# Performance work log

Measured on AMD Instinct MI355X. Metric: run time of the kernel, lower is better.

Reference implementation:

```python
import jax, jax.numpy as jnp
import numpy as np

V, D, H, L, FF, NC = 32000, 512, 8, 4, 2048, 10
HD = D // H
EPS = 1e-5


def _layernorm(x, g, b):
    m = jnp.mean(x, axis=-1, keepdims=True)
    v = jnp.mean((x - m) ** 2, axis=-1, keepdims=True)
    return (x - m) * jax.lax.rsqrt(v + EPS) * g + b


def _pos_encoding(T, d):
    pos = jnp.arange(T, dtype=jnp.float32)[:, None]
    div = jnp.exp(jnp.arange(0, d, 2, dtype=jnp.float32) * (-np.log(10000.0) / d))
    pe = jnp.zeros((T, d), dtype=jnp.float32)
    pe = pe.at[:, 0::2].set(jnp.sin(pos * div))
    pe = pe.at[:, 1::2].set(jnp.cos(pos * div))
    return pe


def setup_inputs() -> dict:
    key = jax.random.key(0)
    ks = iter(jax.random.split(key, 32))
    n = lambda shape, s=0.02: jax.random.normal(next(ks), shape, dtype=jnp.float32) * s
    inp = {
        "tokens": jax.random.randint(next(ks), (8, 1024), 0, V),
        "emb": n((V, D), 1.0),
        # attention projections, stored (in, out) so y = x @ W + b
        "Wq": n((L, D, D)), "bq": jnp.zeros((L, D)),
        "Wk": n((L, D, D)), "bk": jnp.zeros((L, D)),
        "Wv": n((L, D, D)), "bv": jnp.zeros((L, D)),
        "Wo": n((L, D, D)), "bo": jnp.zeros((L, D)),
        "ln1_g": jnp.ones((L, D)), "ln1_b": jnp.zeros((L, D)),
        "ln2_g": jnp.ones((L, D)), "ln2_b": jnp.zeros((L, D)),
        "W1": n((L, D, FF)), "b1": jnp.zeros((L, FF)),
        "W2": n((L, FF, D)), "b2": jnp.zeros((L, D)),
        "heavy_w": n((D, D)), "heavy_b": jnp.zeros((D,)),
        "heavy_a1": n((D, D)), "heavy_a2": n((D, D)),
        "norm_g": jnp.ones((D,)), "norm_b": jnp.zeros((D,)),
        "cls_W": n((D, NC)), "cls_b": jnp.zeros((NC,)),
    }
    return inp


def reference(tokens, emb, Wq, bq, Wk, bk, Wv, bv, Wo, bo,
              ln1_g, ln1_b, ln2_g, ln2_b, W1, b1, W2, b2,
              heavy_w, heavy_b, heavy_a1, heavy_a2,
              norm_g, norm_b, cls_W, cls_b):
    B, T = tokens.shape
    x = emb[tokens] + _pos_encoding(T, D)[None]  # [B,T,D]
    scale = 1.0 / np.sqrt(HD)
    for l in range(L):
        # attention block (pre-norm)
        h = _layernorm(x, ln1_g[l], ln1_b[l])
        q = (h @ Wq[l] + bq[l]).reshape(B, T, H, HD)
        k = (h @ Wk[l] + bk[l]).reshape(B, T, H, HD)
        v = (h @ Wv[l] + bv[l]).reshape(B, T, H, HD)
        scores = jnp.einsum("bqhd,bkhd->bhqk", q, k) * scale
        attn = jax.nn.softmax(scores, axis=-1)
        o = jnp.einsum("bhqk,bkhd->bqhd", attn, v).reshape(B, T, D)
        x = x + (o @ Wo[l] + bo[l])
        # feedforward block
        h = _layernorm(x, ln2_g[l], ln2_b[l])
        x = x + (jax.nn.gelu(h @ W1[l] + b1[l], approximate=False) @ W2[l] + b2[l])
    # heavy layer: chained matmuls + bias + tanh (vectorized over B*T)
    x = jnp.tanh(((x @ heavy_w) @ heavy_a1) @ heavy_a2 + heavy_b)
    x = _layernorm(x, norm_g, norm_b)
    x = jnp.mean(x, axis=1)  # [B,D]
    return x @ cls_W + cls_b  # [B,NC]
```

## Files before the change

### kernel.cpp

```cpp
#include <hip/hip_runtime.h>
#include <math.h>

#define BS   8
#define TT   1024
#define DD   512
#define HH   8
#define LL   4
#define FFD  2048
#define NCC  10
#define MM   (BS*TT)
#define MDl  ((long)MM*DD)

typedef unsigned short u16;
typedef short  short8 __attribute__((ext_vector_type(8)));
typedef float  f32x4  __attribute__((ext_vector_type(4)));
typedef u16    u16x8  __attribute__((ext_vector_type(8)));
typedef u16    u16x4  __attribute__((ext_vector_type(4)));

static __device__ __forceinline__ u16 f2b(float f) {
    union { float f; unsigned u; } x; x.f = f;
    unsigned r = x.u + 0x7FFFu + ((x.u >> 16) & 1u);
    return (u16)(r >> 16);
}
static __device__ __forceinline__ u16 f2b_fast(float f) {
    union { float f; unsigned u; } x; x.f = f;
    return (u16)((x.u + 0x8000u) >> 16);
}
static __device__ __forceinline__ float b2f(u16 u) {
    union { unsigned u; float f; } x; x.u = ((unsigned)u) << 16;
    return x.f;
}

__global__ __launch_bounds__(256)
void embed_kernel(const int* __restrict__ tok, const float* __restrict__ emb,
                  float* __restrict__ X) {
    int i = blockIdx.x * 256 + threadIdx.x;
    int d = i & (DD - 1);
    int row = i >> 9;
    int t = row & (TT - 1);
    int j = d >> 1;
    float freq = __expf((float)(2 * j) * (-9.210340371976184f / 512.0f));
    float ang = (float)t * freq;
    float pe = (d & 1) ? cosf(ang) : sinf(ang);
    X[i] = emb[(long)tok[row] * DD + d] + pe;
}

template<int OUTBF>
__global__ __launch_bounds__(256)
void ln_kernel(const float* __restrict__ in, void* __restrict__ outp,
               const float* __restrict__ g, const float* __restrict__ b) {
    int row = blockIdx.x;
    int tid = threadIdx.x;
    const float* x = in + (long)row * DD;
    float x1 = x[tid], x2 = x[tid + 256];
    __shared__ float red[256], red2[256];
    red[tid] = x1 + x2;
    red2[tid] = x1 * x1 + x2 * x2;
    __syncthreads();
    for (int st = 128; st > 0; st >>= 1) {
        if (tid < st) { red[tid] += red[tid + st]; red2[tid] += red2[tid + st]; }
        __syncthreads();
    }
    float mean = red[0] * (1.0f / DD);
    float var = red2[0] * (1.0f / DD) - mean * mean;
    float rstd = rsqrtf(var + 1e-5f);
    float y1 = (x1 - mean) * rstd * g[tid] + b[tid];
    float y2 = (x2 - mean) * rstd * g[tid + 256] + b[tid + 256];
    if (OUTBF) {
        u16* o = (u16*)outp + (long)row * DD;
        o[tid] = f2b(y1); o[tid + 256] = f2b(y2);
    } else {
        float* o = (float*)outp + (long)row * DD;
        o[tid] = y1; o[tid + 256] = y2;
    }
}

template<int OUTBF, int HAS_BIAS, int ACT, int HAS_RES>
__global__ __launch_bounds__(512, 2)
void mfma_gemm(const u16* __restrict__ A, const u16* __restrict__ BT,
               const float* __restrict__ bias, const float* __restrict__ R,
               void* __restrict__ Cout, int N, int K) {
    __shared__ __align__(16) u16 lds[17408];
    u16* As = lds;
    u16* Bs = lds + 8192;
    const int tid = threadIdx.x;
    const int lane = tid & 63;
    const int w = tid >> 6;
    const int wm = w >> 1;
    const int wn = w & 1;
    const long bm = (long)blockIdx.y * 128;
    const long bn = (long)blockIdx.x * 128;

    f32x4 acc[2][4];
#pragma unroll
    for (int i = 0; i < 2; ++i)
#pragma unroll
        for (int j = 0; j < 4; ++j) acc[i][j] = {0.f, 0.f, 0.f, 0.f};

    const int srow = tid >> 2;
    const int sc0 = (tid & 3) * 2;
    const u16* Ag = A + (bm + srow) * K + sc0 * 8;
    const u16* Bg = BT + (bn + srow) * K + sc0 * 8;
    int soff[2];
#pragma unroll
    for (int j = 0; j < 2; ++j)
        soff[j] = srow * 64 + ((sc0 + j) ^ (srow & 7)) * 8;

    const int fr = lane & 15;
    const int g = lane >> 4;
    const int am0 = wm * 32 + fr;
    const int bn0 = wn * 64 + fr;
    const int sw = fr & 7;

    u16x8 sa[2][2], sb[2][2];
#pragma unroll
    for (int j = 0; j < 2; ++j) {
        sa[0][j] = *(const u16x8*)(Ag + j * 8);
        sb[0][j] = *(const u16x8*)(Bg + j * 8);
    }

    for (int k0 = 0; k0 < K; k0 += 128) {
#pragma unroll
        for (int half = 0; half < 2; ++half) {
            const int cb = half, nb = half ^ 1;
            __syncthreads();
#pragma unroll
            for (int j = 0; j < 2; ++j) {
                *(u16x8*)&As[soff[j]] = sa[cb][j];
                *(u16x8*)&Bs[soff[j]] = sb[cb][j];
            }
            const int knext = k0 + (half + 1) * 64;
            if (knext < K) {
#pragma unroll
                for (int j = 0; j < 2; ++j) {
                    sa[nb][j] = *(const u16x8*)(Ag + knext + j * 8);
                    sb[nb][j] = *(const u16x8*)(Bg + knext + j * 8);
                }
            }
            __syncthreads();
#pragma unroll
            for (int kk = 0; kk < 2; ++kk) {
                const int pos = ((kk << 2) + g) ^ sw;
                short8 af[2], bfv[4];
#pragma unroll
                for (int mi = 0; mi < 2; ++mi)
                    af[mi] = *(const short8*)&As[(am0 + mi * 16) * 64 + pos * 8];
#pragma unroll
                for (int ni = 0; ni < 4; ++ni)
                    bfv[ni] = *(const short8*)&Bs[(bn0 + ni * 16) * 64 + pos * 8];
#pragma unroll
                for (int mi = 0; mi < 2; ++mi)
#pragma unroll
                    for (int ni = 0; ni < 4; ++ni)
                        acc[mi][ni] = __builtin_amdgcn_mfma_f32_16x16x32_bf16(
                            af[mi], bfv[ni], acc[mi][ni], 0, 0, 0);
            }
        }
    }

    const int erow0 = wm * 32 + g * 4;
    const int ecol0 = wn * 64 + fr;

    if (OUTBF) {
        __syncthreads();
#pragma unroll
        for (int ni = 0; ni < 4; ++ni) {
            const long col = bn + ecol0 + ni * 16;
            float bv = 0.f;
            if (HAS_BIAS) bv = bias[col];
#pragma unroll
            for (int mi = 0; mi < 2; ++mi)
#pragma unroll
                for (int r = 0; r < 4; ++r) {
                    const int row = erow0 + mi * 16 + r;
                    float v = acc[mi][ni][r];
                    if (HAS_BIAS) v += bv;
                    if (ACT == 1) v = 0.5f * v * (1.0f + erff(v * 0.70710678118654752f));
                    if (ACT == 2) v = tanhf(v);
                    if (HAS_RES) v += R[(bm + row) * N + col];
                    lds[row * 136 + ecol0 + ni * 16] = f2b(v);
                }
        }
        __syncthreads();
        const int srow2 = tid >> 4;
        const int sch2 = tid & 15;
        u16* Cp = (u16*)Cout;
#pragma unroll
        for (int rr = 0; rr < 4; ++rr) {
            const int row = srow2 + rr * 32;
            u16x8 vv = *(const u16x8*)&lds[row * 136 + sch2 * 8];
            *(u16x8*)(Cp + (bm + row) * N + bn + sch2 * 8) = vv;
        }
    } else {
#pragma unroll
        for (int ni = 0; ni < 4; ++ni) {
            const long col = bn + ecol0 + ni * 16;
            float bv = 0.f;
            if (HAS_BIAS) bv = bias[col];
#pragma unroll
            for (int mi = 0; mi < 2; ++mi)
#pragma unroll
                for (int r = 0; r < 4; ++r) {
                    const long row = bm + erow0 + mi * 16 + r;
                    float v = acc[mi][ni][r];
                    if (HAS_BIAS) v += bv;
                    if (ACT == 1) v = 0.5f * v * (1.0f + erff(v * 0.70710678118654752f));
                    if (ACT == 2) v = tanhf(v);
                    if (HAS_RES) v += R[row * N + col];
                    ((float*)Cout)[row * N + col] = v;
                }
        }
    }
}

__global__ __launch_bounds__(256, 2)
void attn_kernel(const u16* __restrict__ QKV, u16* __restrict__ O) {
    const int qblk = blockIdx.x;
    const int h = blockIdx.y;
    const int b = blockIdx.z;
    const int tid = threadIdx.x;
    const int lane = tid & 63;
    const int w = tid >> 6;
    const int fr = lane & 15;
    const int g = lane >> 4;
    const int q8 = g * 8;

    __shared__ __align__(16) u16 Ks[64 * 64];
    __shared__ __align__(16) u16 Vt[64 * 72];
    __shared__ __align__(16) u16 Pw[4][32 * 72];

    const long rowb = (long)b * TT;
    const int wq0 = qblk * 128 + w * 32;

    short8 qf[2][2];
#pragma unroll
    for (int qt = 0; qt < 2; ++qt)
#pragma unroll
        for (int hf = 0; hf < 2; ++hf)
            qf[qt][hf] = *(const short8*)(QKV + (rowb + wq0 + qt * 16 + fr) * 1536
                                          + h * 64 + hf * 32 + q8);

    f32x4 accO[2][4];
    float lsum[2][4];
#pragma unroll
    for (int qt = 0; qt < 2; ++qt) {
#pragma unroll
        for (int nt = 0; nt < 4; ++nt) accO[qt][nt] = {0.f, 0.f, 0.f, 0.f};
#pragma unroll
        for (int r = 0; r < 4; ++r) lsum[qt][r] = 0.f;
    }

    const int skey = tid >> 2;
    const int skc = (tid & 3) * 2;
    const int koff0 = skey * 64 + ((skc ^ (skey & 7)) * 8);
    const int koff1 = skey * 64 + (((skc + 1) ^ (skey & 7)) * 8);
    const int vkp = tid & 31;
    const int vd0 = (tid >> 5) * 8;

    auto load_kv = [&](int kt_, u16x8* kr_, u16x8* vr_) {
        const long tb_ = (rowb + (long)kt_ * 64) * 1536 + h * 64;
        const u16* kp_ = QKV + tb_ + 512 + (long)skey * 1536 + skc * 8;
        kr_[0] = *(const u16x8*)kp_;
        kr_[1] = *(const u16x8*)(kp_ + 8);
        const u16* vp_ = QKV + tb_ + 1024 + (long)(vkp * 2) * 1536 + vd0;
        vr_[0] = *(const u16x8*)vp_;
        vr_[1] = *(const u16x8*)(vp_ + 1536);
    };
    auto stage = [&](u16x8* kr_, u16x8* vr_) {
        *(u16x8*)&Ks[koff0] = kr_[0];
        *(u16x8*)&Ks[koff1] = kr_[1];
        unsigned* Vt32 = (unsigned*)Vt;
#pragma unroll
        for (int j = 0; j < 8; ++j)
            Vt32[(vd0 + j) * 36 + vkp] =
                (unsigned)vr_[0][j] | ((unsigned)vr_[1][j] << 16);
    };
    auto compute = [&]() {
        f32x4 accS[2][4];
#pragma unroll
        for (int qt = 0; qt < 2; ++qt)
#pragma unroll
            for (int n = 0; n < 4; ++n) accS[qt][n] = {0.f, 0.f, 0.f, 0.f};
#pragma unroll
        for (int n = 0; n < 4; ++n)
#pragma unroll
            for (int hf = 0; hf < 2; ++hf) {
                short8 bk = *(const short8*)&Ks[(n * 16 + fr) * 64
                                                + ((((hf << 2) + g) ^ (fr & 7)) * 8)];
                accS[0][n] = __builtin_amdgcn_mfma_f32_16x16x32_bf16(qf[0][hf], bk, accS[0][n], 0, 0, 0);
                accS[1][n] = __builtin_amdgcn_mfma_f32_16x16x32_bf16(qf[1][hf], bk, accS[1][n], 0, 0, 0);
            }
#pragma unroll
        for (int qt = 0; qt < 2; ++qt)
#pragma unroll
            for (int r = 0; r < 4; ++r) {
                int prow = qt * 16 + g * 4 + r;
#pragma unroll
                for (int n = 0; n < 4; ++n) {
                    float pv = exp2f(accS[qt][n][r] * 0.18033688011112042f);
                    lsum[qt][r] += pv;
                    Pw[w][prow * 72 + n * 16 + fr] = f2b_fast(pv);
                }
            }
#pragma unroll
        for (int hf = 0; hf < 2; ++hf) {
            short8 pa0 = *(const short8*)&Pw[w][fr * 72 + hf * 32 + q8];
            short8 pa1 = *(const short8*)&Pw[w][(16 + fr) * 72 + hf * 32 + q8];
#pragma unroll
            for (int nt = 0; nt < 4; ++nt) {
                short8 bv = *(const short8*)&Vt[(nt * 16 + fr) * 72 + hf * 32 + q8];
                accO[0][nt] = __builtin_amdgcn_mfma_f32_16x16x32_bf16(pa0, bv, accO[0][nt], 0, 0, 0);
                accO[1][nt] = __builtin_amdgcn_mfma_f32_16x16x32_bf16(pa1, bv, accO[1][nt], 0, 0, 0);
            }
        }
    };

    u16x8 krA[2], vrA[2], krB[2], vrB[2];
    load_kv(0, krA, vrA);

#pragma unroll 1
    for (int kt = 0; kt < 16; kt += 2) {
        __syncthreads();
        stage(krA, vrA);
        load_kv(kt + 1, krB, vrB);
        __syncthreads();
        compute();
        __syncthreads();
        stage(krB, vrB);
        if (kt + 2 < 16) load_kv(kt + 2, krA, vrA);
        __syncthreads();
        compute();
    }

#pragma unroll
    for (int qt = 0; qt < 2; ++qt)
#pragma unroll
        for (int r = 0; r < 4; ++r) {
            float s = lsum[qt][r];
            s += __shfl_xor(s, 1, 64);
            s += __shfl_xor(s, 2, 64);
            s += __shfl_xor(s, 4, 64);
            s += __shfl_xor(s, 8, 64);
            lsum[qt][r] = 1.0f / s;
        }
#pragma unroll
    for (int qt = 0; qt < 2; ++qt)
#pragma unroll
        for (int nt = 0; nt < 4; ++nt)
#pragma unroll
            for (int r = 0; r < 4; ++r) {
                long row = rowb + wq0 + qt * 16 + g * 4 + r;
                O[row * DD + h * 64 + nt * 16 + fr] = f2b(accO[qt][nt][r] * lsum[qt][r]);
            }
}

struct WP   { const float* s; u16* d; };
struct WTbl { WP e[19]; };

__global__ __launch_bounds__(256)
void wprep512_kernel(WTbl tbl) {
    const float* src = tbl.e[blockIdx.z].s;
    u16* dst = tbl.e[blockIdx.z].d;
    int k0 = blockIdx.y * 32, n0 = blockIdx.x * 32;
    __shared__ float tile[32][33];
    int tx = threadIdx.x & 31, ty = threadIdx.x >> 5;
#pragma unroll
    for (int i = 0; i < 4; ++i)
        tile[ty + 8 * i][tx] = src[(long)(k0 + ty + 8 * i) * 512 + n0 + tx];
    __syncthreads();
#pragma unroll
    for (int i = 0; i < 4; ++i) {
        int r = ty + 8 * i;
        dst[(long)(n0 + r) * 512 + k0 + tx] = f2b(tile[tx][r]);
    }
}

__global__ __launch_bounds__(256)
void wprep_kernel(const float* __restrict__ src, u16* __restrict__ dst,
                  int K, int N, long srcLS, long dstLS) {
    int l = blockIdx.z;
    src += (long)l * srcLS;
    dst += (long)l * dstLS;
    int k0 = blockIdx.y * 32, n0 = blockIdx.x * 32;
    __shared__ float tile[32][33];
    int tx = threadIdx.x & 31, ty = threadIdx.x >> 5;
#pragma unroll
    for (int i = 0; i < 4; ++i)
        tile[ty + 8 * i][tx] = src[(long)(k0 + ty + 8 * i) * N + n0 + tx];
    __syncthreads();
#pragma unroll
    for (int i = 0; i < 4; ++i) {
        int r = ty + 8 * i;
        dst[(long)(n0 + r) * K + k0 + tx] = f2b(tile[tx][r]);
    }
}

__global__ __launch_bounds__(256)
void bprep_kernel(const float* __restrict__ bq, const float* __restrict__ bk,
                  const float* __restrict__ bv, float* __restrict__ dst) {
    int i = blockIdx.x * 256 + threadIdx.x;
    int l = i / 1536, j = i - l * 1536;
    float v = (j < 512) ? bq[l * 512 + j]
            : (j < 1024) ? bk[l * 512 + j - 512]
                         : bv[l * 512 + j - 1024];
    dst[i] = v;
}

__global__ __launch_bounds__(256)
void f2b_kernel(const float* __restrict__ in, u16* __restrict__ out, int n) {
    int i = blockIdx.x * 256 + threadIdx.x;
    if (i < n) out[i] = f2b(in[i]);
}

__global__ __launch_bounds__(256)
void zero_kernel(float* __restrict__ p, int n) {
    int i = blockIdx.x * 256 + threadIdx.x;
    if (i < n) p[i] = 0.0f;
}

__global__ __launch_bounds__(256)
void colmean_kernel(const float* __restrict__ Hn, float* __restrict__ XM) {
    int blk = blockIdx.x;
    int b = blk >> 5;
    int r0 = (blk & 31) * 32;
    int tid = threadIdx.x;
    float acc0 = 0.0f, acc1 = 0.0f;
    for (int r = 0; r < 32; ++r) {
        long off = ((long)b * TT + r0 + r) * DD + tid;
        acc0 += Hn[off];
        acc1 += Hn[off + 256];
    }
    atomicAdd(&XM[b * DD + tid], acc0);
    atomicAdd(&XM[b * DD + tid + 256], acc1);
}

__global__ __launch_bounds__(256)
void cls_kernel(const float* __restrict__ XM, const float* __restrict__ W,
                const float* __restrict__ bias, float* __restrict__ out) {
    int b = blockIdx.x;
    int tid = threadIdx.x;
    __shared__ float xm[DD];
    xm[tid] = XM[b * DD + tid] * (1.0f / TT);
    xm[tid + 256] = XM[b * DD + tid + 256] * (1.0f / TT);
    __syncthreads();
    if (tid < NCC) {
        float s = bias[tid];
        for (int d = 0; d < DD; ++d) s += xm[d] * W[d * NCC + tid];
        out[b * NCC + tid] = s;
    }
}

extern "C" void kernel_launch(void* const* d_in, const int* in_sizes, int n_in,
                              void* d_out, int out_size, void* d_ws, size_t ws_size,
                              hipStream_t stream) {
    const int*   tokens  = (const int*)d_in[0];
    const float* emb     = (const float*)d_in[1];
    const float* Wq      = (const float*)d_in[2];
    const float* bq      = (const float*)d_in[3];
    const float* Wk      = (const float*)d_in[4];
    const float* bk      = (const float*)d_in[5];
    const float* Wv      = (const float*)d_in[6];
    const float* bv      = (const float*)d_in[7];
    const float* Wo      = (const float*)d_in[8];
    const float* bo      = (const float*)d_in[9];
    const float* ln1_g   = (const float*)d_in[10];
    const float* ln1_b   = (const float*)d_in[11];
    const float* ln2_g   = (const float*)d_in[12];
    const float* ln2_b   = (const float*)d_in[13];
    const float* W1      = (const float*)d_in[14];
    const float* b1      = (const float*)d_in[15];
    const float* W2      = (const float*)d_in[16];
    const float* b2      = (const float*)d_in[17];
    const float* heavy_w = (const float*)d_in[18];
    const float* heavy_b = (const float*)d_in[19];
    const float* heavy_a1= (const float*)d_in[20];
    const float* heavy_a2= (const float*)d_in[21];
    const float* norm_g  = (const float*)d_in[22];
    const float* norm_b  = (const float*)d_in[23];
    const float* cls_W   = (const float*)d_in[24];
    const float* cls_b   = (const float*)d_in[25];
    float* out = (float*)d_out;

    char* p = (char*)d_ws;
    float* X    = (float*)p;  p += MDl * 4;
    u16*   Hh   = (u16*)p;    p += MDl * 2;
    u16*   QKVb = (u16*)p;
    u16*   FFb  = QKVb;
    u16*   T1   = QKVb;
    u16*   T2   = QKVb + MDl;
    float* LNout= (float*)QKVb;
    p += (long)MM * 1536 * 2;
    u16*   Ob   = (u16*)p;    p += MDl * 2;
    u16*   Xbf  = (u16*)p;    p += MDl * 2;
    u16*   WqkvT= (u16*)p;    p += 4L * 1536 * 512 * 2;
    u16*   WoT  = (u16*)p;    p += 4L * 512 * 512 * 2;
    u16*   W1T  = (u16*)p;    p += 4L * 2048 * 512 * 2;
    u16*   W2T  = (u16*)p;    p += 4L * 512 * 2048 * 2;
    u16*   WhT  = (u16*)p;    p += 3L * 512 * 512 * 2;
    float* bqkv = (float*)p;  p += 4L * 1536 * 4;
    float* XM   = (float*)p;  p += (long)BS * DD * 4;

    dim3 blk(256);
    dim3 blk512(512);

    WTbl tbl;
    for (int l = 0; l < 4; ++l) {
        tbl.e[l * 4 + 0] = {Wq + (long)l * 262144, WqkvT + (long)l * 786432};
        tbl.e[l * 4 + 1] = {Wk + (long)l * 262144, WqkvT + (long)l * 786432 + 262144};
        tbl.e[l * 4 + 2] = {Wv + (long)l * 262144, WqkvT + (long)l * 786432 + 524288};
        tbl.e[l * 4 + 3] = {Wo + (long)l * 262144, WoT + (long)l * 262144};
    }
    tbl.e[16] = {heavy_w,  WhT};
    tbl.e[17] = {heavy_a1, WhT + 262144};
    tbl.e[18] = {heavy_a2, WhT + 524288};
    wprep512_kernel<<<dim3(16, 16, 19), blk, 0, stream>>>(tbl);
    wprep_kernel<<<dim3(64, 16, 4), blk, 0, stream>>>(W1, W1T,  512, 2048, 1048576, 1048576);
    wprep_kernel<<<dim3(16, 64, 4), blk, 0, stream>>>(W2, W2T, 2048,  512, 1048576, 1048576);
    bprep_kernel<<<24, blk, 0, stream>>>(bq, bk, bv, bqkv);

    embed_kernel<<<MM * DD / 256, blk, 0, stream>>>(tokens, emb, X);

    dim3 gQKV(12, 64), g512(4, 64), gFF1(16, 64);

    for (int l = 0; l < LL; ++l) {
        ln_kernel<1><<<MM, blk, 0, stream>>>(X, Hh, ln1_g + l * DD, ln1_b + l * DD);
        mfma_gemm<1, 1, 0, 0><<<gQKV, blk512, 0, stream>>>(
            Hh, WqkvT + (long)l * 786432, bqkv + l * 1536, nullptr, QKVb, 1536, 512);
        attn_kernel<<<dim3(8, HH, BS), blk, 0, stream>>>(QKVb, Ob);
        mfma_gemm<0, 1, 0, 1><<<g512, blk512, 0, stream>>>(
            Ob, WoT + (long)l * 262144, bo + l * DD, X, X, 512, 512);
        ln_kernel<1><<<MM, blk, 0, stream>>>(X, Hh, ln2_g + l * DD, ln2_b + l * DD);
        mfma_gemm<1, 1, 1, 0><<<gFF1, blk512, 0, stream>>>(
            Hh, W1T + (long)l * 1048576, b1 + l * FFD, nullptr, FFb, 2048, 512);
        mfma_gemm<0, 1, 0, 1><<<g512, blk512, 0, stream>>>(
            FFb, W2T + (long)l * 1048576, b2 + l * DD, X, X, 512, 2048);
    }

    f2b_kernel<<<MM * DD / 256, blk, 0, stream>>>(X, Xbf, MM * DD);
    mfma_gemm<1, 0, 0, 0><<<g512, blk512, 0, stream>>>(Xbf, WhT,          nullptr, nullptr, T1, 512, 512);
    mfma_gemm<1, 0, 0, 0><<<g512, blk512, 0, stream>>>(T1,  WhT + 262144, nullptr, nullptr, T2, 512, 512);
    mfma_gemm<0, 1, 2, 0><<<g512, blk512, 0, stream>>>(T2,  WhT + 524288, heavy_b, nullptr, X,  512, 512);

    ln_kernel<0><<<MM, blk, 0, stream>>>(X, LNout, norm_g, norm_b);
    zero_kernel<<<(BS * DD + 255) / 256, blk, 0, stream>>>(XM, BS * DD);
    colmean_kernel<<<256, blk, 0, stream>>>(LNout, XM);
    cls_kernel<<<BS, blk, 0, stream>>>(XM, cls_W, cls_b, out);
}
```

Measured before the change: 857.0 us.

## Shrink attention query tile to 64 rows and remap grid for K/V locality

The attention kernel now gives each wave 16 query rows instead of 32, so a block covers 64 queries and the grid grows from 512 to 1024 blocks. A 1D block index is decoded so that consecutive blocks share the same batch/head group of 8, which keeps the K/V reads for one head close together in time and in cache. Launch bounds are raised to allow 4 blocks per CU, and the per-wave P scratch in shared memory is halved. This gives more blocks in flight for latency hiding, at the cost of each block reloading the full K/V for half as many queries, so K/V traffic per query doubles.

```diff
diff --git a/kernel.cpp b/kernel.cpp
--- a/kernel.cpp
+++ b/kernel.cpp
@@ -213,11 +213,13 @@
     }
 }
 
-__global__ __launch_bounds__(256, 2)
+__global__ __launch_bounds__(256, 4)
 void attn_kernel(const u16* __restrict__ QKV, u16* __restrict__ O) {
-    const int qblk = blockIdx.x;
-    const int h = blockIdx.y;
-    const int b = blockIdx.z;
+    const int id = blockIdx.x;
+    const int bh = ((id >> 7) << 3) | (id & 7);
+    const int qblk = (id >> 3) & 15;
+    const int h = bh & 7;
+    const int b = bh >> 3;
     const int tid = threadIdx.x;
     const int lane = tid & 63;
     const int w = tid >> 6;
@@ -227,28 +229,23 @@
 
     __shared__ __align__(16) u16 Ks[64 * 64];
     __shared__ __align__(16) u16 Vt[64 * 72];
-    __shared__ __align__(16) u16 Pw[4][32 * 72];
+    __shared__ __align__(16) u16 Pw[4][16 * 72];
 
     const long rowb = (long)b * TT;
-    const int wq0 = qblk * 128 + w * 32;
-
-    short8 qf[2][2];
-#pragma unroll
-    for (int qt = 0; qt < 2; ++qt)
-#pragma unroll
-        for (int hf = 0; hf < 2; ++hf)
-            qf[qt][hf] = *(const short8*)(QKV + (rowb + wq0 + qt * 16 + fr) * 1536
-                                          + h * 64 + hf * 32 + q8);
-
-    f32x4 accO[2][4];
-    float lsum[2][4];
-#pragma unroll
-    for (int qt = 0; qt < 2; ++qt) {
-#pragma unroll
-        for (int nt = 0; nt < 4; ++nt) accO[qt][nt] = {0.f, 0.f, 0.f, 0.f};
-#pragma unroll
-        for (int r = 0; r < 4; ++r) lsum[qt][r] = 0.f;
-    }
+    const int wq0 = qblk * 64 + w * 16;
+
+    short8 qf[2];
+#pragma unroll
+    for (int hf = 0; hf < 2; ++hf)
+        qf[hf] = *(const short8*)(QKV + (rowb + wq0 + fr) * 1536
+                                  + h * 64 + hf * 32 + q8);
+
+    f32x4 accO[4];
+    float lsum[4];
+#pragma unroll
+    for (int nt = 0; nt < 4; ++nt) accO[nt] = {0.f, 0.f, 0.f, 0.f};
+#pragma unroll
+    for (int r = 0; r < 4; ++r) lsum[r] = 0.f;
 
     const int skey = tid >> 2;
     const int skc = (tid & 3) * 2;
@@ -276,41 +273,34 @@
                 (unsigned)vr_[0][j] | ((unsigned)vr_[1][j] << 16);
     };
     auto compute = [&]() {
-        f32x4 accS[2][4];
-#pragma unroll
-        for (int qt = 0; qt < 2; ++qt)
-#pragma unroll
-            for (int n = 0; n < 4; ++n) accS[qt][n] = {0.f, 0.f, 0.f, 0.f};
+        f32x4 accS[4];
+#pragma unroll
+        for (int n = 0; n < 4; ++n) accS[n] = {0.f, 0.f, 0.f, 0.f};
 #pragma unroll
         for (int n = 0; n < 4; ++n)
 #pragma unroll
             for (int hf = 0; hf < 2; ++hf) {
                 short8 bk = *(const short8*)&Ks[(n * 16 + fr) * 64
                                                 + ((((hf << 2) + g) ^ (fr & 7)) * 8)];
-                accS[0][n] = __builtin_amdgcn_mfma_f32_16x16x32_bf16(qf[0][hf], bk, accS[0][n], 0, 0, 0);
-                accS[1][n] = __builtin_amdgcn_mfma_f32_16x16x32_bf16(qf[1][hf], bk, accS[1][n], 0, 0, 0);
+                accS[n] = __builtin_amdgcn_mfma_f32_16x16x32_bf16(qf[hf], bk, accS[n], 0, 0, 0);
             }
 #pragma unroll
-        for (int qt = 0; qt < 2; ++qt)
-#pragma unroll
-            for (int r = 0; r < 4; ++r) {
-                int prow = qt * 16 + g * 4 + r;
-#pragma unroll
-                for (int n = 0; n < 4; ++n) {
-                    float pv = exp2f(accS[qt][n][r] * 0.18033688011112042f);
-                    lsum[qt][r] += pv;
-                    Pw[w][prow * 72 + n * 16 + fr] = f2b_fast(pv);
-                }
+        for (int r = 0; r < 4; ++r) {
+            int prow = g * 4 + r;
+#pragma unroll
+            for (int n = 0; n < 4; ++n) {
+                float pv = exp2f(accS[n][r] * 0.18033688011112042f);
+                lsum[r] += pv;
+                Pw[w][prow * 72 + n * 16 + fr] = f2b_fast(pv);
             }
+        }
 #pragma unroll
         for (int hf = 0; hf < 2; ++hf) {
-            short8 pa0 = *(const short8*)&Pw[w][fr * 72 + hf * 32 + q8];
-            short8 pa1 = *(const short8*)&Pw[w][(16 + fr) * 72 + hf * 32 + q8];
+            short8 pa = *(const short8*)&Pw[w][fr * 72 + hf * 32 + q8];
 #pragma unroll
             for (int nt = 0; nt < 4; ++nt) {
                 short8 bv = *(const short8*)&Vt[(nt * 16 + fr) * 72 + hf * 32 + q8];
-                accO[0][nt] = __builtin_amdgcn_mfma_f32_16x16x32_bf16(pa0, bv, accO[0][nt], 0, 0, 0);
-                accO[1][nt] = __builtin_amdgcn_mfma_f32_16x16x32_bf16(pa1, bv, accO[1][nt], 0, 0, 0);
+                accO[nt] = __builtin_amdgcn_mfma_f32_16x16x32_bf16(pa, bv, accO[nt], 0, 0, 0);
             }
         }
     };
@@ -333,25 +323,21 @@
     }
 
 #pragma unroll
-    for (int qt = 0; qt < 2; ++qt)
+    for (int r = 0; r < 4; ++r) {
+        float s = lsum[r];
+        s += __shfl_xor(s, 1, 64);
+        s += __shfl_xor(s, 2, 64);
+        s += __shfl_xor(s, 4, 64);
+        s += __shfl_xor(s, 8, 64);
+        lsum[r] = 1.0f / s;
+    }
+#pragma unroll
+    for (int nt = 0; nt < 4; ++nt)
 #pragma unroll
         for (int r = 0; r < 4; ++r) {
-            float s = lsum[qt][r];
-            s += __shfl_xor(s, 1, 64);
-            s += __shfl_xor(s, 2, 64);
-            s += __shfl_xor(s, 4, 64);
-            s += __shfl_xor(s, 8, 64);
-            lsum[qt][r] = 1.0f / s;
-        }
-#pragma unroll
-    for (int qt = 0; qt < 2; ++qt)
-#pragma unroll
-        for (int nt = 0; nt < 4; ++nt)
-#pragma unroll
-            for (int r = 0; r < 4; ++r) {
-                long row = rowb + wq0 + qt * 16 + g * 4 + r;
-                O[row * DD + h * 64 + nt * 16 + fr] = f2b(accO[qt][nt][r] * lsum[qt][r]);
-            }
+            long row = rowb + wq0 + g * 4 + r;
+            O[row * DD + h * 64 + nt * 16 + fr] = f2b(accO[nt][r] * lsum[r]);
+        }
 }
 
 struct WP   { const float* s; u16* d; };
@@ -526,7 +512,7 @@
         ln_kernel<1><<<MM, blk, 0, stream>>>(X, Hh, ln1_g + l * DD, ln1_b + l * DD);
         mfma_gemm<1, 1, 0, 0><<<gQKV, blk512, 0, stream>>>(
             Hh, WqkvT + (long)l * 786432, bqkv + l * 1536, nullptr, QKVb, 1536, 512);
-        attn_kernel<<<dim3(8, HH, BS), blk, 0, stream>>>(QKVb, Ob);
+        attn_kernel<<<dim3(1024), blk, 0, stream>>>(QKVb, Ob);
         mfma_gemm<0, 1, 0, 1><<<g512, blk512, 0, stream>>>(
             Ob, WoT + (long)l * 262144, bo + l * DD, X, X, 512, 512);
         ln_kernel<1><<<MM, blk, 0, stream>>>(X, Hh, ln2_g + l * DD, ln2_b + l * DD);
```

New measurement: 888.7 us. 1.04x slower.

## Load GEMM tiles directly into LDS with global_load_lds instead of register staging

Applied to the files above, without the earlier changes.

Replaces the register-staged, software double-buffered global-to-LDS copy in the bf16 GEMM with direct global_load_lds transfers. The swizzle moves into the global address selection, so each wave writes a contiguous 512-element LDS span that still matches the XOR-swizzled read pattern. This removes the VGPR round trip and the LDS store instructions. It also drops the register prefetch, so loads for the next k-tile no longer overlap the current tile's MFMAs, and every 64-wide k step now waits on two barriers.

```diff
diff --git a/kernel.cpp b/kernel.cpp
--- a/kernel.cpp
+++ b/kernel.cpp
@@ -97,14 +97,17 @@
 #pragma unroll
         for (int j = 0; j < 4; ++j) acc[i][j] = {0.f, 0.f, 0.f, 0.f};
 
-    const int srow = tid >> 2;
-    const int sc0 = (tid & 3) * 2;
-    const u16* Ag = A + (bm + srow) * K + sc0 * 8;
-    const u16* Bg = BT + (bn + srow) * K + sc0 * 8;
-    int soff[2];
-#pragma unroll
-    for (int j = 0; j < 2; ++j)
-        soff[j] = srow * 64 + ((sc0 + j) ^ (srow & 7)) * 8;
+    const int l8 = lane >> 3;
+    const int chunk = (lane & 7) ^ l8;
+    const int row0 = w * 8 + l8;
+    const u16* Ag0 = A  + (bm + row0) * K + chunk * 8;
+    const u16* Ag1 = A  + (bm + row0 + 64) * K + chunk * 8;
+    const u16* Bg0 = BT + (bn + row0) * K + chunk * 8;
+    const u16* Bg1 = BT + (bn + row0 + 64) * K + chunk * 8;
+    u16* dA0 = As + w * 512;
+    u16* dA1 = As + 4096 + w * 512;
+    u16* dB0 = Bs + w * 512;
+    u16* dB1 = Bs + 4096 + w * 512;
 
     const int fr = lane & 15;
     const int g = lane >> 4;
@@ -112,49 +115,37 @@
     const int bn0 = wn * 64 + fr;
     const int sw = fr & 7;
 
-    u16x8 sa[2][2], sb[2][2];
-#pragma unroll
-    for (int j = 0; j < 2; ++j) {
-        sa[0][j] = *(const u16x8*)(Ag + j * 8);
-        sb[0][j] = *(const u16x8*)(Bg + j * 8);
-    }
-
-    for (int k0 = 0; k0 < K; k0 += 128) {
-#pragma unroll
-        for (int half = 0; half < 2; ++half) {
-            const int cb = half, nb = half ^ 1;
-            __syncthreads();
-#pragma unroll
-            for (int j = 0; j < 2; ++j) {
-                *(u16x8*)&As[soff[j]] = sa[cb][j];
-                *(u16x8*)&Bs[soff[j]] = sb[cb][j];
-            }
-            const int knext = k0 + (half + 1) * 64;
-            if (knext < K) {
-#pragma unroll
-                for (int j = 0; j < 2; ++j) {
-                    sa[nb][j] = *(const u16x8*)(Ag + knext + j * 8);
-                    sb[nb][j] = *(const u16x8*)(Bg + knext + j * 8);
-                }
-            }
-            __syncthreads();
-#pragma unroll
-            for (int kk = 0; kk < 2; ++kk) {
-                const int pos = ((kk << 2) + g) ^ sw;
-                short8 af[2], bfv[4];
-#pragma unroll
-                for (int mi = 0; mi < 2; ++mi)
-                    af[mi] = *(const short8*)&As[(am0 + mi * 16) * 64 + pos * 8];
+    for (int k0 = 0; k0 < K; k0 += 64) {
+        __syncthreads();
+        __builtin_amdgcn_global_load_lds(
+            (const __attribute__((address_space(1))) void*)(Ag0 + k0),
+            (__attribute__((address_space(3))) void*)dA0, 16, 0, 0);
+        __builtin_amdgcn_global_load_lds(
+            (const __attribute__((address_space(1))) void*)(Ag1 + k0),
+            (__attribute__((address_space(3))) void*)dA1, 16, 0, 0);
+        __builtin_amdgcn_global_load_lds(
+            (const __attribute__((address_space(1))) void*)(Bg0 + k0),
+            (__attribute__((address_space(3))) void*)dB0, 16, 0, 0);
+        __builtin_amdgcn_global_load_lds(
+            (const __attribute__((address_space(1))) void*)(Bg1 + k0),
+            (__attribute__((address_space(3))) void*)dB1, 16, 0, 0);
+        __syncthreads();
+#pragma unroll
+        for (int kk = 0; kk < 2; ++kk) {
+            const int pos = ((kk << 2) + g) ^ sw;
+            short8 af[2], bfv[4];
+#pragma unroll
+            for (int mi = 0; mi < 2; ++mi)
+                af[mi] = *(const short8*)&As[(am0 + mi * 16) * 64 + pos * 8];
+#pragma unroll
+            for (int ni = 0; ni < 4; ++ni)
+                bfv[ni] = *(const short8*)&Bs[(bn0 + ni * 16) * 64 + pos * 8];
+#pragma unroll
+            for (int mi = 0; mi < 2; ++mi)
 #pragma unroll
                 for (int ni = 0; ni < 4; ++ni)
-                    bfv[ni] = *(const short8*)&Bs[(bn0 + ni * 16) * 64 + pos * 8];
-#pragma unroll
-                for (int mi = 0; mi < 2; ++mi)
-#pragma unroll
-                    for (int ni = 0; ni < 4; ++ni)
-                        acc[mi][ni] = __builtin_amdgcn_mfma_f32_16x16x32_bf16(
-                            af[mi], bfv[ni], acc[mi][ni], 0, 0, 0);
-            }
+                    acc[mi][ni] = __builtin_amdgcn_mfma_f32_16x16x32_bf16(
+                        af[mi], bfv[ni], acc[mi][ni], 0, 0, 0);
         }
     }
 
```

After: 966.3 us. 1.13x slower.
